# Kernel tuning notes

Hardware: AMD Instinct MI355X
Metric: run time of the kernel (lower is better)

The kernel has to match this reference:

```python
import jax, jax.numpy as jnp
import numpy as np

N_ANGLES = 180
N_DETECTORS = 256


def _bilinear_sample(img, x, y):
    """Bilinear sample img[y, x]; zero outside. img: [H, W]; x, y: any shape."""
    H, W = img.shape
    x0 = jnp.floor(x)
    y0 = jnp.floor(y)
    xi = x0.astype(jnp.int32)
    yi = y0.astype(jnp.int32)
    wx = x - x0
    wy = y - y0

    def get(ix, iy):
        valid = (ix >= 0) & (ix < W) & (iy >= 0) & (iy < H)
        ixc = jnp.clip(ix, 0, W - 1)
        iyc = jnp.clip(iy, 0, H - 1)
        return jnp.where(valid, img[iyc, ixc], jnp.zeros((), img.dtype))

    v00 = get(xi, yi)
    v01 = get(xi + 1, yi)
    v10 = get(xi, yi + 1)
    v11 = get(xi + 1, yi + 1)
    return (v00 * (1.0 - wx) + v01 * wx) * (1.0 - wy) + (v10 * (1.0 - wx) + v11 * wx) * wy


def setup_inputs() -> dict:
    key = jax.random.key(0)
    inputs = jax.random.uniform(key, (8, 256, 256, 1), dtype=jnp.float32)
    return {"inputs": inputs}


def reference(inputs):
    # Parallel-beam forward Radon transform (forwardproject).
    # inputs: [B, H, W, 1] image batch -> sinogram [B, n_angles, n_detectors, 1]
    B, H, W, _ = inputs.shape
    A, D = N_ANGLES, N_DETECTORS
    T = H  # integration samples along each ray

    theta = jnp.linspace(0.0, jnp.pi, A, endpoint=False, dtype=inputs.dtype)
    cos_t = jnp.cos(theta)[:, None, None]  # [A,1,1]
    sin_t = jnp.sin(theta)[:, None, None]

    s = (jnp.arange(D, dtype=inputs.dtype) - (D - 1) / 2.0)[None, :, None]  # detector offsets
    t = (jnp.arange(T, dtype=inputs.dtype) - (T - 1) / 2.0)[None, None, :]  # along-ray offsets

    cx = (W - 1) / 2.0
    cy = (H - 1) / 2.0
    # sample coords for every (angle, detector, ray-step): [A, D, T]
    x = cx + s * cos_t - t * sin_t
    y = cy + s * sin_t + t * cos_t

    imgs = inputs[..., 0]  # [B, H, W]
    vals = jax.vmap(lambda im: _bilinear_sample(im, x, y))(imgs)  # [B, A, D, T]
    sino = vals.sum(axis=-1)  # ray integral (unit step length)
    return sino[..., None]  # [B, A, D, 1]
```

## Files before the change

kernel.cpp:

```cpp
#include <hip/hip_runtime.h>
#include <math.h>

#define NA    180
#define HB    8
#define KB    33
#define PC    262
#define PR    266
#define TROWS 9
#define TSZ   (PC * TROWS)
#define OUTN  (8 * NA * 256)
#define APG   2
#define NGY   46
#define NGX   45

typedef _Float16 h2  __attribute__((ext_vector_type(2)));
typedef _Float16 h8  __attribute__((ext_vector_type(8)));
typedef __fp16   hf2 __attribute__((ext_vector_type(2)));

__device__ __forceinline__ h2 pkrtz(float a, float b) {
    hf2 t = __builtin_amdgcn_cvt_pkrtz(a, b);
    return __builtin_bit_cast(h2, t);
}
__device__ __forceinline__ float fdot2f(h2 a, h2 b, float c) {
#if __has_builtin(__builtin_amdgcn_fdot2)
    return __builtin_amdgcn_fdot2(__builtin_bit_cast(hf2, a),
                                  __builtin_bit_cast(hf2, b), c, false);
#else
    return c + (float)a.x * (float)b.x + (float)a.y * (float)b.y;
#endif
}
__device__ __forceinline__ float imc(const float* im, int y, int x) {
    return ((unsigned)y < 256u && (unsigned)x < 256u) ? im[(y << 8) + x] : 0.0f;
}

__global__ __launch_bounds__(256) void prep_kernel(
    const float* __restrict__ img, uint4* __restrict__ P0,
    uint4* __restrict__ P1, float* __restrict__ out, float* __restrict__ tab)
{
    const int tid = threadIdx.x;
    const int row = blockIdx.x;
    const int mb  = blockIdx.y;

    if (mb == 0) {
        for (int i = row * 256 + tid; i < OUTN; i += PR * 256) out[i] = 0.0f;
    }
    if (mb == 1 && row == 0 && tid < NA) {
        const float theta = (float)tid * ((float)M_PI / (float)NA);
        tab[tid]      = cosf(theta);
        tab[tid + NA] = sinf(theta);
    }

    const int v = row - 3;
    uint4* dst = (mb == 0 ? P0 : P1) + (size_t)row * PC;
    for (int j = tid; j < PC; j += 256) {
        const int u = j - 2;
        h8 t = {};
        if (j < 261) {
            if (mb == 0) {
                #pragma unroll
                for (int b = 0; b < 8; ++b)
                    t[b] = (_Float16)imc(img + ((size_t)b << 16), v, u);
            } else {
                #pragma unroll
                for (int b = 0; b < 8; ++b)
                    t[b] = (_Float16)imc(img + ((size_t)b << 16), u, v);
            }
        }
        dst[j] = __builtin_bit_cast(uint4, t);
    }
}

#define SAMPLE8(JV, UV, VPV, ACC)                                             \
    {                                                                         \
        const float ucl = fminf(fmaxf((UV), -1.5f), 257.5f);                  \
        const float uf = floorf(ucl);                                         \
        const float wu = ucl - uf;                                            \
        float vf = floorf(VPV);                                               \
        vf = fminf(fmaxf(vf, 0.0f), 7.0f);                                    \
        const float wv = (VPV) - vf;                                          \
        const int idx = (int)fmaf(vf, (float)PC, uf) + 2;                     \
        const h8 ra0 = __builtin_bit_cast(h8, s_tile[idx]);                   \
        const h8 ra1 = __builtin_bit_cast(h8, s_tile[idx + 1]);               \
        const h8 rb0 = __builtin_bit_cast(h8, s_tile[idx + PC]);              \
        const h8 rb1 = __builtin_bit_cast(h8, s_tile[idx + PC + 1]);          \
        const h2 wv2 = pkrtz(wv, wv);                                         \
        const h8 wv8 = __builtin_shufflevector(wv2, wv2, 0,1,0,1,0,1,0,1);    \
        const h8 v0 = (rb0 - ra0) * wv8 + ra0;                                \
        const h8 v1 = (rb1 - ra1) * wv8 + ra1;                                \
        h2 wu2 = pkrtz(1.0f - wu, wu);                                        \
        wu2 = ((unsigned)(JV) < span) ? wu2 : hz;                             \
        ACC[0] = fdot2f(__builtin_shufflevector(v0, v1, 0,  8), wu2, ACC[0]); \
        ACC[1] = fdot2f(__builtin_shufflevector(v0, v1, 1,  9), wu2, ACC[1]); \
        ACC[2] = fdot2f(__builtin_shufflevector(v0, v1, 2, 10), wu2, ACC[2]); \
        ACC[3] = fdot2f(__builtin_shufflevector(v0, v1, 3, 11), wu2, ACC[3]); \
        ACC[4] = fdot2f(__builtin_shufflevector(v0, v1, 4, 12), wu2, ACC[4]); \
        ACC[5] = fdot2f(__builtin_shufflevector(v0, v1, 5, 13), wu2, ACC[5]); \
        ACC[6] = fdot2f(__builtin_shufflevector(v0, v1, 6, 14), wu2, ACC[6]); \
        ACC[7] = fdot2f(__builtin_shufflevector(v0, v1, 7, 15), wu2, ACC[7]); \
    }

template<bool MODEX>
__device__ __forceinline__ void radon_body(
    const uint4* __restrict__ Pbase,
    float* __restrict__ out, const float* __restrict__ tab,
    uint4* s_tile, int tid, int p, int gi)
{
    const int lo = -2 + p * HB;

    {
        const uint4* src = Pbase + (size_t)(lo + 3) * PC;
        for (int i = tid; i < TSZ; i += 256) s_tile[i] = src[i];
    }
    __syncthreads();

    const float detf = (float)tid - 127.5f;
    const float lof = (float)lo;
    const h2 hz = {};

    for (int g = 0; g < APG; ++g) {
        const int ai = gi * APG + g;
        int a;
        if (MODEX) { if (ai >= 89) break; a = 46 + ai; }
        else       { if (ai >= 91) break; a = (ai <= 45) ? ai : 89 + ai; }

        const float c = tab[a];
        const float s = tab[a + NA];

        const float xc = 127.5f + detf * c + 127.5f * s;
        const float yc = 127.5f + detf * s - 127.5f * c;

        const float ucst = MODEX ? yc : xc;
        const float vcst = MODEX ? xc : yc;
        const float du   = MODEX ? c  : -s;
        const float dv   = MODEX ? -s : c;

        const float vlo_f = fmaxf(lof, -1.0f);
        const float vhi_f = fminf(lof + (float)HB, 256.0f);
        const float inv = 1.0f / dv;
        const float f1 = (vlo_f - vcst) * inv;
        const float f2 = (vhi_f - vcst) * inv;
        const float fmn = fminf(f1, f2);
        const float fmx = fmaxf(f1, f2);
        int kmin, kend;
        if (dv > 0.0f) { kmin = (int)ceilf(fmn);      kend = (int)ceilf(fmx); }
        else           { kmin = (int)floorf(fmn) + 1; kend = (int)floorf(fmx) + 1; }

        const int len = kend - kmin;
        const int jlo = max(0, -kmin);
        const int jhi = min(len, 256 - kmin);
        const int spani = max(0, jhi - jlo);

        int m = spani;
        m = max(m, __shfl_xor(m, 1));
        m = max(m, __shfl_xor(m, 2));
        m = max(m, __shfl_xor(m, 4));
        m = max(m, __shfl_xor(m, 8));
        m = max(m, __shfl_xor(m, 16));
        m = max(m, __shfl_xor(m, 32));
        const int mspan = __builtin_amdgcn_readfirstlane(m);
        if (mspan <= 0) continue;
        const unsigned span = (unsigned)spani;

        const int kstart = kmin + jlo;

        float u  = fmaf((float)kstart, du, ucst);
        float vp = fmaf((float)kstart, dv, vcst - lof);
        const float du2 = du + du, dv2 = dv + dv;
        const float du3 = du2 + du, dv3 = dv2 + dv;
        const float du4 = du2 + du2, dv4 = dv2 + dv2;

        float accA[8] = {}, accB[8] = {}, accC[8] = {}, accD[8] = {};

        int j = 0;
        for (; j + 3 < mspan; j += 4) {
            SAMPLE8(j,     u,       vp,       accA);
            SAMPLE8(j + 1, u + du,  vp + dv,  accB);
            SAMPLE8(j + 2, u + du2, vp + dv2, accC);
            SAMPLE8(j + 3, u + du3, vp + dv3, accD);
            u += du4; vp += dv4;
        }
        for (; j + 1 < mspan; j += 2) {
            SAMPLE8(j,     u,      vp,      accA);
            SAMPLE8(j + 1, u + du, vp + dv, accB);
            u += du2; vp += dv2;
        }
        if (j < mspan) SAMPLE8(j, u, vp, accA);

        if (spani > 0) {
            float* o = &out[(a << 8) + tid];
            #pragma unroll
            for (int b = 0; b < 8; ++b)
                atomicAdd(o + b * (NA << 8),
                          (accA[b] + accC[b]) + (accB[b] + accD[b]));
        }
    }
}

__global__ __launch_bounds__(256, 4) void radon_kernel(
    const uint4* __restrict__ P0, const uint4* __restrict__ P1,
    float* __restrict__ out, const float* __restrict__ tab)
{
    __shared__ uint4 s_tile[TSZ];
    const int tid = threadIdx.x;
    const int p   = blockIdx.x;
    const int gid = blockIdx.y;
    if (gid < NGY)
        radon_body<false>(P0, out, tab, s_tile, tid, p, gid);
    else
        radon_body<true >(P1, out, tab, s_tile, tid, p, gid - NGY);
}

extern "C" void kernel_launch(void* const* d_in, const int* in_sizes, int n_in,
                              void* d_out, int out_size, void* d_ws, size_t ws_size,
                              hipStream_t stream) {
    const float* img = (const float*)d_in[0];
    float* out = (float*)d_out;

    uint4* P0 = (uint4*)d_ws;
    uint4* P1 = P0 + (size_t)PR * PC;
    float* tab = (float*)(P1 + (size_t)PR * PC);

    prep_kernel<<<dim3(PR, 2), 256, 0, stream>>>(img, P0, P1, out, tab);
    radon_kernel<<<dim3(KB, NGY + NGX), 256, 0, stream>>>(P0, P1, out, tab);
}
```

Before: 107.4 us.

## Replace LDS row-band tiling with per-angle ray chunks reading global memory

Removes the shared-memory tile of image rows and the band decomposition. Each block now handles one angle and one of 12 chunks of the ray, clips the ray to the image box, and gathers bilinear samples straight from the padded fp16 global arrays. This drops the tile loads, the barrier and the per-band clipping overhead, and lowers atomic count (180x12 blocks instead of 33 bands). The cost is that all sample gathers now go through L1/L2 instead of LDS.

```diff
diff --git a/kernel.cpp b/kernel.cpp
--- a/kernel.cpp
+++ b/kernel.cpp
@@ -2,16 +2,10 @@
 #include <math.h>
 
 #define NA    180
-#define HB    8
-#define KB    33
 #define PC    262
 #define PR    266
-#define TROWS 9
-#define TSZ   (PC * TROWS)
 #define OUTN  (8 * NA * 256)
-#define APG   2
-#define NGY   46
-#define NGX   45
+#define NCH   12
 
 typedef _Float16 h2  __attribute__((ext_vector_type(2)));
 typedef _Float16 h8  __attribute__((ext_vector_type(8)));
@@ -70,25 +64,25 @@
     }
 }
 
-#define SAMPLE8(JV, UV, VPV, ACC)                                             \
+#define SAMPLE8G(JV, UV, VPV, ACC)                                            \
     {                                                                         \
         const float ucl = fminf(fmaxf((UV), -1.5f), 257.5f);                  \
         const float uf = floorf(ucl);                                         \
         const float wu = ucl - uf;                                            \
         float vf = floorf(VPV);                                               \
-        vf = fminf(fmaxf(vf, 0.0f), 7.0f);                                    \
+        vf = fminf(fmaxf(vf, -2.0f), 258.0f);                                 \
         const float wv = (VPV) - vf;                                          \
-        const int idx = (int)fmaf(vf, (float)PC, uf) + 2;                     \
-        const h8 ra0 = __builtin_bit_cast(h8, s_tile[idx]);                   \
-        const h8 ra1 = __builtin_bit_cast(h8, s_tile[idx + 1]);               \
-        const h8 rb0 = __builtin_bit_cast(h8, s_tile[idx + PC]);              \
-        const h8 rb1 = __builtin_bit_cast(h8, s_tile[idx + PC + 1]);          \
+        const int idx = (int)fmaf(vf, (float)PC, uf) + (3 * PC + 2);          \
+        const h8 ra0 = __builtin_bit_cast(h8, P[idx]);                        \
+        const h8 ra1 = __builtin_bit_cast(h8, P[idx + 1]);                    \
+        const h8 rb0 = __builtin_bit_cast(h8, P[idx + PC]);                   \
+        const h8 rb1 = __builtin_bit_cast(h8, P[idx + PC + 1]);               \
         const h2 wv2 = pkrtz(wv, wv);                                         \
         const h8 wv8 = __builtin_shufflevector(wv2, wv2, 0,1,0,1,0,1,0,1);    \
         const h8 v0 = (rb0 - ra0) * wv8 + ra0;                                \
         const h8 v1 = (rb1 - ra1) * wv8 + ra1;                                \
         h2 wu2 = pkrtz(1.0f - wu, wu);                                        \
-        wu2 = ((unsigned)(JV) < span) ? wu2 : hz;                             \
+        wu2 = ((unsigned)(JV) < uspan) ? wu2 : hz;                            \
         ACC[0] = fdot2f(__builtin_shufflevector(v0, v1, 0,  8), wu2, ACC[0]); \
         ACC[1] = fdot2f(__builtin_shufflevector(v0, v1, 1,  9), wu2, ACC[1]); \
         ACC[2] = fdot2f(__builtin_shufflevector(v0, v1, 2, 10), wu2, ACC[2]); \
@@ -100,99 +94,80 @@
     }
 
 template<bool MODEX>
-__device__ __forceinline__ void radon_body(
-    const uint4* __restrict__ Pbase,
+__device__ __forceinline__ void radon_ray(
+    const uint4* __restrict__ P,
     float* __restrict__ out, const float* __restrict__ tab,
-    uint4* s_tile, int tid, int p, int gi)
+    int tid, int a, int chunk)
 {
-    const int lo = -2 + p * HB;
+    const float c = tab[a];
+    const float s = tab[a + NA];
+    const float detf = (float)tid - 127.5f;
 
-    {
-        const uint4* src = Pbase + (size_t)(lo + 3) * PC;
-        for (int i = tid; i < TSZ; i += 256) s_tile[i] = src[i];
-    }
-    __syncthreads();
+    const float xc = 127.5f + detf * c + 127.5f * s;
+    const float yc = 127.5f + detf * s - 127.5f * c;
 
-    const float detf = (float)tid - 127.5f;
-    const float lof = (float)lo;
+    const float ucst = MODEX ? yc : xc;
+    const float vcst = MODEX ? xc : yc;
+    const float du   = MODEX ? c  : -s;
+    const float dv   = MODEX ? -s : c;
+
+    const float iv = 1.0f / dv;
+    const float va = (-1.0f - vcst) * iv, vb = (256.0f - vcst) * iv;
+    const float iu = 1.0f / du;
+    const float ua = (-1.0f - ucst) * iu, ub = (256.0f - ucst) * iu;
+    float lo = fmaxf(fminf(va, vb), fminf(ua, ub));
+    float hi = fminf(fmaxf(va, vb), fmaxf(ua, ub));
+    lo = fminf(fmaxf(lo, 0.0f), 512.0f);
+    hi = fminf(fmaxf(hi, -1.0f), 256.0f);
+    const int kmin = (int)ceilf(lo);
+    const int kend = min(256, (int)floorf(hi) + 1);
+    const int len  = max(0, kend - kmin);
+
+    const int clen = (len + (NCH - 1)) / NCH;
+    const int k0   = kmin + chunk * clen;
+    const int span = min(clen, kend - k0);
+
+    int m = span;
+    m = max(m, __shfl_xor(m, 1));
+    m = max(m, __shfl_xor(m, 2));
+    m = max(m, __shfl_xor(m, 4));
+    m = max(m, __shfl_xor(m, 8));
+    m = max(m, __shfl_xor(m, 16));
+    m = max(m, __shfl_xor(m, 32));
+    const int mspan = __builtin_amdgcn_readfirstlane(m);
+    if (mspan <= 0) return;
+    const unsigned uspan = (unsigned)max(span, 0);
     const h2 hz = {};
 
-    for (int g = 0; g < APG; ++g) {
-        const int ai = gi * APG + g;
-        int a;
-        if (MODEX) { if (ai >= 89) break; a = 46 + ai; }
-        else       { if (ai >= 91) break; a = (ai <= 45) ? ai : 89 + ai; }
+    float u  = fmaf((float)k0, du, ucst);
+    float vp = fmaf((float)k0, dv, vcst);
+    const float du2 = du + du, dv2 = dv + dv;
+    const float du3 = du2 + du, dv3 = dv2 + dv;
+    const float du4 = du2 + du2, dv4 = dv2 + dv2;
 
-        const float c = tab[a];
-        const float s = tab[a + NA];
+    float accA[8] = {}, accB[8] = {}, accC[8] = {}, accD[8] = {};
 
-        const float xc = 127.5f + detf * c + 127.5f * s;
-        const float yc = 127.5f + detf * s - 127.5f * c;
+    int j = 0;
+    for (; j + 3 < mspan; j += 4) {
+        SAMPLE8G(j,     u,       vp,       accA);
+        SAMPLE8G(j + 1, u + du,  vp + dv,  accB);
+        SAMPLE8G(j + 2, u + du2, vp + dv2, accC);
+        SAMPLE8G(j + 3, u + du3, vp + dv3, accD);
+        u += du4; vp += dv4;
+    }
+    for (; j + 1 < mspan; j += 2) {
+        SAMPLE8G(j,     u,      vp,      accA);
+        SAMPLE8G(j + 1, u + du, vp + dv, accB);
+        u += du2; vp += dv2;
+    }
+    if (j < mspan) SAMPLE8G(j, u, vp, accA);
 
-        const float ucst = MODEX ? yc : xc;
-        const float vcst = MODEX ? xc : yc;
-        const float du   = MODEX ? c  : -s;
-        const float dv   = MODEX ? -s : c;
-
-        const float vlo_f = fmaxf(lof, -1.0f);
-        const float vhi_f = fminf(lof + (float)HB, 256.0f);
-        const float inv = 1.0f / dv;
-        const float f1 = (vlo_f - vcst) * inv;
-        const float f2 = (vhi_f - vcst) * inv;
-        const float fmn = fminf(f1, f2);
-        const float fmx = fmaxf(f1, f2);
-        int kmin, kend;
-        if (dv > 0.0f) { kmin = (int)ceilf(fmn);      kend = (int)ceilf(fmx); }
-        else           { kmin = (int)floorf(fmn) + 1; kend = (int)floorf(fmx) + 1; }
-
-        const int len = kend - kmin;
-        const int jlo = max(0, -kmin);
-        const int jhi = min(len, 256 - kmin);
-        const int spani = max(0, jhi - jlo);
-
-        int m = spani;
-        m = max(m, __shfl_xor(m, 1));
-        m = max(m, __shfl_xor(m, 2));
-        m = max(m, __shfl_xor(m, 4));
-        m = max(m, __shfl_xor(m, 8));
-        m = max(m, __shfl_xor(m, 16));
-        m = max(m, __shfl_xor(m, 32));
-        const int mspan = __builtin_amdgcn_readfirstlane(m);
-        if (mspan <= 0) continue;
-        const unsigned span = (unsigned)spani;
-
-        const int kstart = kmin + jlo;
-
-        float u  = fmaf((float)kstart, du, ucst);
-        float vp = fmaf((float)kstart, dv, vcst - lof);
-        const float du2 = du + du, dv2 = dv + dv;
-        const float du3 = du2 + du, dv3 = dv2 + dv;
-        const float du4 = du2 + du2, dv4 = dv2 + dv2;
-
-        float accA[8] = {}, accB[8] = {}, accC[8] = {}, accD[8] = {};
-
-        int j = 0;
-        for (; j + 3 < mspan; j += 4) {
-            SAMPLE8(j,     u,       vp,       accA);
-            SAMPLE8(j + 1, u + du,  vp + dv,  accB);
-            SAMPLE8(j + 2, u + du2, vp + dv2, accC);
-            SAMPLE8(j + 3, u + du3, vp + dv3, accD);
-            u += du4; vp += dv4;
-        }
-        for (; j + 1 < mspan; j += 2) {
-            SAMPLE8(j,     u,      vp,      accA);
-            SAMPLE8(j + 1, u + du, vp + dv, accB);
-            u += du2; vp += dv2;
-        }
-        if (j < mspan) SAMPLE8(j, u, vp, accA);
-
-        if (spani > 0) {
-            float* o = &out[(a << 8) + tid];
-            #pragma unroll
-            for (int b = 0; b < 8; ++b)
-                atomicAdd(o + b * (NA << 8),
-                          (accA[b] + accC[b]) + (accB[b] + accD[b]));
-        }
+    if (span > 0) {
+        float* o = &out[(a << 8) + tid];
+        #pragma unroll
+        for (int b = 0; b < 8; ++b)
+            atomicAdd(o + b * (NA << 8),
+                      (accA[b] + accC[b]) + (accB[b] + accD[b]));
     }
 }
 
@@ -200,14 +175,12 @@
     const uint4* __restrict__ P0, const uint4* __restrict__ P1,
     float* __restrict__ out, const float* __restrict__ tab)
 {
-    __shared__ uint4 s_tile[TSZ];
-    const int tid = threadIdx.x;
-    const int p   = blockIdx.x;
-    const int gid = blockIdx.y;
-    if (gid < NGY)
-        radon_body<false>(P0, out, tab, s_tile, tid, p, gid);
+    const int a     = blockIdx.x;
+    const int chunk = blockIdx.y;
+    if (a >= 46 && a < 135)
+        radon_ray<true >(P1, out, tab, threadIdx.x, a, chunk);
     else
-        radon_body<true >(P1, out, tab, s_tile, tid, p, gid - NGY);
+        radon_ray<false>(P0, out, tab, threadIdx.x, a, chunk);
 }
 
 extern "C" void kernel_launch(void* const* d_in, const int* in_sizes, int n_in,
@@ -221,5 +194,5 @@
     float* tab = (float*)(P1 + (size_t)PR * PC);
 
     prep_kernel<<<dim3(PR, 2), 256, 0, stream>>>(img, P0, P1, out, tab);
-    radon_kernel<<<dim3(KB, NGY + NGX), 256, 0, stream>>>(P0, P1, out, tab);
+    radon_kernel<<<dim3(NA, NCH), 256, 0, stream>>>(P0, P1, out, tab);
 }
```

Result: slower. 118.7 us (+10.5%).
